# Kernel optimization log

Measured on AMD Instinct MI355X. Metric: run time of the kernel, lower is better.

Reference implementation:

```python
import jax, jax.numpy as jnp
import numpy as np

B, S, H, NH = 2, 2048, 2048, 16
HD = H // NH  # 128
NEG = -1e9


def setup_inputs() -> dict:
    key = jax.random.key(0)
    ks = jax.random.split(key, 5)
    hidden_states = jax.random.normal(ks[0], (B, S, H), dtype=jnp.float32)
    causal = jnp.tril(jnp.ones((S, S), dtype=bool))
    attention_mask = jnp.where(causal, 0.0, NEG).astype(jnp.float32)[None, None, :, :]
    scale = 0.02
    Wq = jax.random.normal(ks[1], (H, H), dtype=jnp.float32) * scale
    Wk = jax.random.normal(ks[2], (H, H), dtype=jnp.float32) * scale
    Wv = jax.random.normal(ks[3], (H, H), dtype=jnp.float32) * scale
    Wo = jax.random.normal(ks[4], (H, H), dtype=jnp.float32) * scale
    return {"hidden_states": hidden_states, "attention_mask": attention_mask,
            "Wq": Wq, "Wk": Wk, "Wv": Wv, "Wo": Wo}


def reference(hidden_states, attention_mask, Wq, Wk, Wv, Wo):
    # nn.Linear(bias=False): y = x @ W.T
    q = hidden_states @ Wq.T  # [B,S,H]
    k = hidden_states @ Wk.T
    v = hidden_states @ Wv.T
    # [B,S,NH,HD] -> [B,NH,S,HD]
    q = q.reshape(B, S, NH, HD).transpose(0, 2, 1, 3)
    k = k.reshape(B, S, NH, HD).transpose(0, 2, 1, 3)
    v = v.reshape(B, S, NH, HD).transpose(0, 2, 1, 3)
    scaling = HD ** -0.5
    # [B,NH,S,S]
    scores = jnp.einsum('bhqd,bhkd->bhqk', q, k) * scaling + attention_mask
    attn = jax.nn.softmax(scores.astype(jnp.float32), axis=-1).astype(q.dtype)
    out = jnp.einsum('bhqk,bhkd->bhqd', attn, v)  # [B,NH,S,HD]
    out = out.transpose(0, 2, 1, 3).reshape(B, S, H)
    return out @ Wo.T
```

## Files before the change

### kernel.cpp

```cpp
#include <hip/hip_runtime.h>

typedef unsigned short u16;
typedef __bf16 bf16x8 __attribute__((ext_vector_type(8)));
typedef float floatx4 __attribute__((ext_vector_type(4)));

#define B_ 2
#define S_ 2048
#define H_ 2048
#define NH_ 16
#define BS_ 4096
#define QKSTR 4096
#define PSTR 72

#define SCL_Q (0.08838834764831843f * 1.4426950408889634f)

#define PART_CH 4194304
#define LP_CH 32768

__device__ __forceinline__ u16 f2bf(float f) {
  unsigned u = __float_as_uint(f);
  u += 0x7fffu + ((u >> 16) & 1u);
  return (u16)(u >> 16);
}

__device__ __forceinline__ void gl_lds16(const void* g, void* l) {
  __builtin_amdgcn_global_load_lds((__attribute__((address_space(1))) void*)g,
                                   (__attribute__((address_space(3))) void*)l,
                                   16, 0, 0);
}

__device__ __forceinline__ floatx4 mfma16(bf16x8 a, bf16x8 b, floatx4 c) {
  return __builtin_amdgcn_mfma_f32_16x16x32_bf16(a, b, c, 0, 0, 0);
}

__global__ void cast_all(const float* __restrict__ X, const float* __restrict__ Wq,
                         const float* __restrict__ Wk, const float* __restrict__ Wv,
                         const float* __restrict__ Wo, u16* __restrict__ Xb,
                         u16* __restrict__ Wb) {
  const int XG = (BS_ * H_) / 4;
  const int WG = (H_ * H_) / 4;
  int i = blockIdx.x * 256 + threadIdx.x;
  const float* src;
  u16* dst;
  int j;
  if (i < XG) {
    src = X; dst = Xb; j = i;
  } else {
    int t = i - XG;
    int w = t >> 20;
    j = t & (WG - 1);
    src = (w == 0) ? Wq : (w == 1) ? Wk : (w == 2) ? Wv : Wo;
    dst = Wb + (size_t)w * (H_ * (size_t)H_);
  }
  float4 v = ((const float4*)src)[j];
  ushort4 o;
  o.x = f2bf(v.x); o.y = f2bf(v.y); o.z = f2bf(v.z); o.w = f2bf(v.w);
  ((ushort4*)dst)[j] = o;
}

template <bool F32OUT>
__global__ __launch_bounds__(512, 2)
void gemm3(const u16* __restrict__ A, const u16* __restrict__ Bm,
           void* __restrict__ Cp, int N, int K, float scl, int ncut) {
  __shared__ __attribute__((aligned(16))) u16 smem[3 * 24576];
  const int tid = threadIdx.x;
  const int wave = tid >> 6, lane = tid & 63;
  const int laneRow = lane & 15, laneQ = lane >> 4;
  const int rs = laneRow & 7;
  const int bm = blockIdx.y * 128, bn = blockIdx.x * 256;
  const int wm = (wave >> 2) * 64;
  const int wn = (wave & 3) * 64;

  floatx4 acc[4][4] = {};

  const int srow = tid >> 3;
  const int sg = (((tid & 7) ^ (srow & 7)) * 8);
  const u16* Abase = A + (size_t)(bm + srow) * K + sg;
  const u16* Bbase = Bm + (size_t)(bn + srow) * K + sg;
  const int NT = K >> 6;

  auto stage = [&](int buf, int kc) {
    char* base = (char*)smem + buf * 49152 + wave * 1024;
#pragma unroll
    for (int i = 0; i < 2; ++i)
      gl_lds16(Abase + (size_t)(i * 64) * K + kc, base + i * 8192);
#pragma unroll
    for (int j = 0; j < 4; ++j)
      gl_lds16(Bbase + (size_t)(j * 64) * K + kc, base + 16384 + j * 8192);
  };

  stage(0, 0);
  stage(1, 64);

  int cur = 0;
  for (int kt = 0; kt < NT; ++kt) {
    if (kt < NT - 1)
      asm volatile("s_waitcnt vmcnt(6)" ::: "memory");
    else
      asm volatile("s_waitcnt vmcnt(0)" ::: "memory");
    asm volatile("s_barrier" ::: "memory");
    if (kt + 2 < NT) {
      int nb = cur + 2; if (nb >= 3) nb -= 3;
      stage(nb, (kt + 2) << 6);
    }
    __builtin_amdgcn_sched_barrier(0);

    const u16* bp = smem + cur * 24576;
    bf16x8 af[4][2], bf[4][2];
#pragma unroll
    for (int mt = 0; mt < 4; ++mt)
#pragma unroll
      for (int ks = 0; ks < 2; ++ks)
        af[mt][ks] = *(const bf16x8*)&bp[(wm + mt * 16 + laneRow) * 64 +
                                         ((ks * 4 + laneQ) ^ rs) * 8];
#pragma unroll
    for (int nt = 0; nt < 4; ++nt)
#pragma unroll
      for (int ks = 0; ks < 2; ++ks)
        bf[nt][ks] = *(const bf16x8*)&bp[8192 + (wn + nt * 16 + laneRow) * 64 +
                                         ((ks * 4 + laneQ) ^ rs) * 8];
    __builtin_amdgcn_s_setprio(1);
#pragma unroll
    for (int mt = 0; mt < 4; ++mt)
#pragma unroll
      for (int nt = 0; nt < 4; ++nt)
#pragma unroll
        for (int ks = 0; ks < 2; ++ks)
          acc[mt][nt] = mfma16(af[mt][ks], bf[nt][ks], acc[mt][nt]);
    __builtin_amdgcn_s_setprio(0);

    cur += 1; if (cur == 3) cur = 0;
  }

#pragma unroll
  for (int mt = 0; mt < 4; ++mt)
#pragma unroll
    for (int nt = 0; nt < 4; ++nt)
#pragma unroll
      for (int r = 0; r < 4; ++r) {
        int m = bm + wm + mt * 16 + laneQ * 4 + r;
        int n = bn + wn + nt * 16 + laneRow;
        if (F32OUT) {
          ((float*)Cp)[(size_t)m * N + n] = acc[mt][nt][r];
        } else {
          float s = (n < ncut) ? scl : 1.0f;
          ((u16*)Cp)[(size_t)m * N + n] = f2bf(acc[mt][nt][r] * s);
        }
      }
}

__global__ __launch_bounds__(256, 3)
void flash_attn(const u16* __restrict__ QKg, const u16* __restrict__ Vt,
                u16* __restrict__ Og, float* __restrict__ Part,
                float* __restrict__ Lp) {
  __shared__ __attribute__((aligned(16))) u16 smem[64 * 128 + 128 * 64 + 128 * PSTR];
  u16* lK = smem;
  u16* lV = smem + 8192;
  u16* lP = smem + 16384;

  const int tid = threadIdx.x;
  const int wave = tid >> 6, lane = tid & 63;
  const int laneRow = lane & 15, laneQ = lane >> 4;
  const int rs = laneRow & 7;
  const int wq = wave * 32;
  const int bx = blockIdx.x, bh = blockIdx.y;
  const int b = bh >> 4, h = bh & 15;

  int qt, ktBeg, ktEnd, ch;
  if (bx < 16) {
    qt = 15 - (bx >> 1);
    ch = bx & 1;
    ktBeg = ch * (qt + 1);
    ktEnd = ktBeg + (qt + 1);
  } else {
    qt = 23 - bx;
    ch = 0;
    ktBeg = 0;
    ktEnd = 2 * (qt + 1);
  }
  const bool partial = (bx < 16);

  const int c16 = (((tid & 15) ^ ((tid >> 4) & 7)) * 8);
  const int c8s = (((tid & 7) ^ ((tid >> 3) & 7)) * 8);

  {
    const int r = tid >> 4;
    const u16* Qp = QKg + (size_t)(b * S_ + qt * 128 + r) * QKSTR + h * 128 + c16;
    char* ld = (char*)smem + wave * 1024;
#pragma unroll
    for (int i = 0; i < 8; ++i)
      gl_lds16(Qp + (size_t)i * 16 * QKSTR, ld + i * 4096);
  }
  __syncthreads();
  bf16x8 qf[2][4];
#pragma unroll
  for (int mt = 0; mt < 2; ++mt)
#pragma unroll
    for (int ks = 0; ks < 4; ++ks)
      qf[mt][ks] = *(const bf16x8*)&smem[(wq + mt * 16 + laneRow) * 128 +
                                         (((ks * 4 + laneQ) ^ rs) * 8)];

  floatx4 accO[2][8] = {};
  float ps[2][4] = {};

  for (int kt = ktBeg; kt < ktEnd; ++kt) {
    __syncthreads();
    {
      const int r = tid >> 4;
      const u16* Kp = QKg + 2048 + (size_t)(b * S_ + kt * 64 + r) * QKSTR + h * 128 + c16;
      char* ld = (char*)lK + wave * 1024;
#pragma unroll
      for (int i = 0; i < 4; ++i)
        gl_lds16(Kp + (size_t)i * 16 * QKSTR, ld + i * 4096);
    }
    {
      const int r = tid >> 3;
      const u16* Vp = Vt + (size_t)(h * 128 + r) * BS_ + b * S_ + kt * 64 + c8s;
      char* ld = (char*)lV + wave * 1024;
#pragma unroll
      for (int i = 0; i < 4; ++i)
        gl_lds16(Vp + (size_t)i * 32 * BS_, ld + i * 4096);
    }
    __syncthreads();

    floatx4 accS[2][4] = {};
#pragma unroll
    for (int ks = 0; ks < 4; ++ks) {
      bf16x8 kf[4];
#pragma unroll
      for (int nt = 0; nt < 4; ++nt)
        kf[nt] = *(const bf16x8*)&lK[(nt * 16 + laneRow) * 128 +
                                     (((ks * 4 + laneQ) ^ rs) * 8)];
#pragma unroll
      for (int mt = 0; mt < 2; ++mt)
#pragma unroll
        for (int nt = 0; nt < 4; ++nt)
          accS[mt][nt] = mfma16(qf[mt][ks], kf[nt], accS[mt][nt]);
    }
    if (kt * 64 + 63 > qt * 128 + wq) {
#pragma unroll
      for (int mt = 0; mt < 2; ++mt)
#pragma unroll
        for (int r = 0; r < 4; ++r) {
          int q = qt * 128 + wq + mt * 16 + laneQ * 4 + r;
#pragma unroll
          for (int nt = 0; nt < 4; ++nt) {
            int k = kt * 64 + nt * 16 + laneRow;
            if (k > q) accS[mt][nt][r] = -1e30f;
          }
        }
    }

#pragma unroll
    for (int mt = 0; mt < 2; ++mt)
#pragma unroll
      for (int r = 0; r < 4; ++r) {
#pragma unroll
        for (int nt = 0; nt < 4; ++nt) {
          float p = exp2f(accS[mt][nt][r]);
          accS[mt][nt][r] = p;
          ps[mt][r] += p;
        }
      }
#pragma unroll
    for (int mt = 0; mt < 2; ++mt)
#pragma unroll
      for (int nt = 0; nt < 4; ++nt)
#pragma unroll
        for (int r = 0; r < 4; ++r)
          lP[(wq + mt * 16 + laneQ * 4 + r) * PSTR + nt * 16 + laneRow] =
              f2bf(accS[mt][nt][r]);

#pragma unroll
    for (int ks = 0; ks < 2; ++ks) {
      bf16x8 pf[2], vf[8];
#pragma unroll
      for (int mt = 0; mt < 2; ++mt)
        pf[mt] = *(const bf16x8*)&lP[(wq + mt * 16 + laneRow) * PSTR + ks * 32 + laneQ * 8];
#pragma unroll
      for (int nt = 0; nt < 8; ++nt)
        vf[nt] = *(const bf16x8*)&lV[(nt * 16 + laneRow) * 64 +
                                     (((ks * 4 + laneQ) ^ rs) * 8)];
#pragma unroll
      for (int mt = 0; mt < 2; ++mt)
#pragma unroll
        for (int nt = 0; nt < 8; ++nt)
          accO[mt][nt] = mfma16(pf[mt], vf[nt], accO[mt][nt]);
    }
  }

  float li[2][4];
#pragma unroll
  for (int mt = 0; mt < 2; ++mt)
#pragma unroll
    for (int r = 0; r < 4; ++r) {
      float l = ps[mt][r];
#pragma unroll
      for (int off = 1; off < 16; off <<= 1)
        l += __shfl_xor(l, off);
      li[mt][r] = l;
    }

  if (!partial) {
#pragma unroll
    for (int mt = 0; mt < 2; ++mt)
#pragma unroll
      for (int r = 0; r < 4; ++r) {
        float inv = 1.0f / li[mt][r];
        int m = qt * 128 + wq + mt * 16 + laneQ * 4 + r;
#pragma unroll
        for (int nt = 0; nt < 8; ++nt) {
          int n = nt * 16 + laneRow;
          Og[(size_t)(b * S_ + m) * H_ + h * 128 + n] = f2bf(accO[mt][nt][r] * inv);
        }
      }
  } else {
    float* P0 = Part + (size_t)ch * PART_CH;
    float* L0 = Lp + (size_t)ch * LP_CH;
#pragma unroll
    for (int mt = 0; mt < 2; ++mt)
#pragma unroll
      for (int r = 0; r < 4; ++r) {
        int qrow = wq + mt * 16 + laneQ * 4 + r;
        int pIdx = ((qt - 8) * 32 + bh) * 128 + qrow;
        if (laneRow == 0) L0[pIdx] = li[mt][r];
#pragma unroll
        for (int nt = 0; nt < 8; ++nt)
          P0[(size_t)pIdx * 128 + nt * 16 + laneRow] = accO[mt][nt][r];
      }
  }
}

__global__ void combine(const float* __restrict__ Part, const float* __restrict__ Lp,
                        u16* __restrict__ Og) {
  int j = blockIdx.x * 256 + threadIdx.x;
  int e = j * 4;
  int d = e & 127;
  int rowid = e >> 7;
  float4 a = ((const float4*)Part)[j];
  float4 c = ((const float4*)(Part + PART_CH))[j];
  float inv = 1.0f / (Lp[rowid] + Lp[LP_CH + rowid]);
  int q = rowid & 127;
  int bh = (rowid >> 7) & 31;
  int qt = 8 + (rowid >> 12);
  int b = bh >> 4, h = bh & 15;
  int m = qt * 128 + q;
  ushort4 o;
  o.x = f2bf((a.x + c.x) * inv);
  o.y = f2bf((a.y + c.y) * inv);
  o.z = f2bf((a.z + c.z) * inv);
  o.w = f2bf((a.w + c.w) * inv);
  *(ushort4*)&Og[(size_t)(b * S_ + m) * H_ + h * 128 + d] = o;
}

extern "C" void kernel_launch(void* const* d_in, const int* in_sizes, int n_in,
                              void* d_out, int out_size, void* d_ws, size_t ws_size,
                              hipStream_t stream) {
  const float* X  = (const float*)d_in[0];
  const float* Wq = (const float*)d_in[2];
  const float* Wk = (const float*)d_in[3];
  const float* Wv = (const float*)d_in[4];
  const float* Wo = (const float*)d_in[5];

  char* ws = (char*)d_ws;
  u16* Xb  = (u16*)(ws);
  u16* Wqb = (u16*)(ws + (16u << 20));
  u16* Wvb = Wqb + 2 * (size_t)H_ * H_;
  u16* Wob = Wqb + 3 * (size_t)H_ * H_;
  u16* QKb = (u16*)(ws + (48u << 20));
  u16* Vtb = (u16*)(ws + (80u << 20));
  u16* AOb = (u16*)(ws + (96u << 20));
  float* Part = (float*)ws;
  float* Lp   = (float*)(ws + 2u * PART_CH * sizeof(float));

  {
    int groups = (BS_ * H_) / 4 + H_ * H_;
    cast_all<<<groups / 256, 256, 0, stream>>>(X, Wq, Wk, Wv, Wo, Xb, Wqb);
  }

  gemm3<false><<<dim3(16, 32), 512, 0, stream>>>(Xb, Wqb, QKb, 4096, 2048, SCL_Q, 2048);
  gemm3<false><<<dim3(16, 16), 512, 0, stream>>>(Wvb, Xb, Vtb, 4096, 2048, 1.0f, 0);

  flash_attn<<<dim3(24, B_ * NH_), 256, 0, stream>>>(QKb, Vtb, AOb, Part, Lp);
  combine<<<PART_CH / 4 / 256, 256, 0, stream>>>(Part, Lp, AOb);

  gemm3<true><<<dim3(8, 32), 512, 0, stream>>>(AOb, Wob, (float*)d_out, 2048, 2048, 1.0f, 0);
}
```

Before: 395.7 us.

## Double-buffer K tiles in LDS and load V fragments directly from global

K tiles are now double-buffered in shared memory, and the next tile's async global-to-LDS load is issued during the current iteration. This overlaps K fetch with compute and replaces the two barriers per iteration with a single waitcnt plus barrier. V is no longer staged through LDS. Each lane reads its bf16x8 V fragments straight from global memory into registers, which cuts LDS traffic but adds register pressure (16 vectors) and uncoalesced, latency-exposed global loads. The waitcnt vmcnt(0) also waits on those V loads, so they may not overlap as fully as intended.

```diff
diff --git a/kernel.cpp b/kernel.cpp
--- a/kernel.cpp
+++ b/kernel.cpp
@@ -153,9 +153,8 @@
 void flash_attn(const u16* __restrict__ QKg, const u16* __restrict__ Vt,
                 u16* __restrict__ Og, float* __restrict__ Part,
                 float* __restrict__ Lp) {
-  __shared__ __attribute__((aligned(16))) u16 smem[64 * 128 + 128 * 64 + 128 * PSTR];
+  __shared__ __attribute__((aligned(16))) u16 smem[2 * 64 * 128 + 128 * PSTR];
   u16* lK = smem;
-  u16* lV = smem + 8192;
   u16* lP = smem + 16384;
 
   const int tid = threadIdx.x;
@@ -181,11 +180,12 @@
   const bool partial = (bx < 16);
 
   const int c16 = (((tid & 15) ^ ((tid >> 4) & 7)) * 8);
-  const int c8s = (((tid & 7) ^ ((tid >> 3) & 7)) * 8);
+  const int rK = tid >> 4;
+  const u16* KpBase = QKg + 2048 + (size_t)(b * S_ + rK) * QKSTR + h * 128 + c16;
+  const u16* vBase = Vt + (size_t)(h * 128 + laneRow) * BS_ + b * S_ + laneQ * 8;
 
   {
-    const int r = tid >> 4;
-    const u16* Qp = QKg + (size_t)(b * S_ + qt * 128 + r) * QKSTR + h * 128 + c16;
+    const u16* Qp = QKg + (size_t)(b * S_ + qt * 128 + rK) * QKSTR + h * 128 + c16;
     char* ld = (char*)smem + wave * 1024;
 #pragma unroll
     for (int i = 0; i < 8; ++i)
@@ -199,29 +199,23 @@
     for (int ks = 0; ks < 4; ++ks)
       qf[mt][ks] = *(const bf16x8*)&smem[(wq + mt * 16 + laneRow) * 128 +
                                          (((ks * 4 + laneQ) ^ rs) * 8)];
+  __syncthreads();
+
+  {
+    const u16* Kp = KpBase + (size_t)ktBeg * (64 * QKSTR);
+    char* ld = (char*)lK + (ktBeg & 1) * 16384 + wave * 1024;
+#pragma unroll
+    for (int i = 0; i < 4; ++i)
+      gl_lds16(Kp + (size_t)i * 16 * QKSTR, ld + i * 4096);
+  }
 
   floatx4 accO[2][8] = {};
   float ps[2][4] = {};
 
   for (int kt = ktBeg; kt < ktEnd; ++kt) {
-    __syncthreads();
-    {
-      const int r = tid >> 4;
-      const u16* Kp = QKg + 2048 + (size_t)(b * S_ + kt * 64 + r) * QKSTR + h * 128 + c16;
-      char* ld = (char*)lK + wave * 1024;
-#pragma unroll
-      for (int i = 0; i < 4; ++i)
-        gl_lds16(Kp + (size_t)i * 16 * QKSTR, ld + i * 4096);
-    }
-    {
-      const int r = tid >> 3;
-      const u16* Vp = Vt + (size_t)(h * 128 + r) * BS_ + b * S_ + kt * 64 + c8s;
-      char* ld = (char*)lV + wave * 1024;
-#pragma unroll
-      for (int i = 0; i < 4; ++i)
-        gl_lds16(Vp + (size_t)i * 32 * BS_, ld + i * 4096);
-    }
-    __syncthreads();
+    asm volatile("s_waitcnt vmcnt(0)" ::: "memory");
+    asm volatile("s_barrier" ::: "memory");
+    const u16* kb = lK + (kt & 1) * 8192;
 
     floatx4 accS[2][4] = {};
 #pragma unroll
@@ -229,7 +223,7 @@
       bf16x8 kf[4];
 #pragma unroll
       for (int nt = 0; nt < 4; ++nt)
-        kf[nt] = *(const bf16x8*)&lK[(nt * 16 + laneRow) * 128 +
+        kf[nt] = *(const bf16x8*)&kb[(nt * 16 + laneRow) * 128 +
                                      (((ks * 4 + laneQ) ^ rs) * 8)];
 #pragma unroll
       for (int mt = 0; mt < 2; ++mt)
@@ -262,6 +256,25 @@
           ps[mt][r] += p;
         }
       }
+
+    bf16x8 vf[2][8];
+    {
+      const u16* vp = vBase + kt * 64;
+#pragma unroll
+      for (int ks = 0; ks < 2; ++ks)
+#pragma unroll
+        for (int nt = 0; nt < 8; ++nt)
+          vf[ks][nt] = *(const bf16x8*)(vp + (size_t)nt * 16 * BS_ + ks * 32);
+    }
+    if (kt + 1 < ktEnd) {
+      const u16* Kp = KpBase + (size_t)(kt + 1) * (64 * QKSTR);
+      char* ld = (char*)lK + ((kt + 1) & 1) * 16384 + wave * 1024;
+#pragma unroll
+      for (int i = 0; i < 4; ++i)
+        gl_lds16(Kp + (size_t)i * 16 * QKSTR, ld + i * 4096);
+    }
+    __builtin_amdgcn_sched_barrier(0);
+
 #pragma unroll
     for (int mt = 0; mt < 2; ++mt)
 #pragma unroll
@@ -273,19 +286,15 @@
 
 #pragma unroll
     for (int ks = 0; ks < 2; ++ks) {
-      bf16x8 pf[2], vf[8];
+      bf16x8 pf[2];
 #pragma unroll
       for (int mt = 0; mt < 2; ++mt)
         pf[mt] = *(const bf16x8*)&lP[(wq + mt * 16 + laneRow) * PSTR + ks * 32 + laneQ * 8];
 #pragma unroll
-      for (int nt = 0; nt < 8; ++nt)
-        vf[nt] = *(const bf16x8*)&lV[(nt * 16 + laneRow) * 64 +
-                                     (((ks * 4 + laneQ) ^ rs) * 8)];
-#pragma unroll
       for (int mt = 0; mt < 2; ++mt)
 #pragma unroll
         for (int nt = 0; nt < 8; ++nt)
-          accO[mt][nt] = mfma16(pf[mt], vf[nt], accO[mt][nt]);
+          accO[mt][nt] = mfma16(pf[mt], vf[ks][nt], accO[mt][nt]);
     }
   }
 
```

After: 529.7 us. 1.34x slower.
